# Kernel tuning notes

Measured on AMD Instinct MI355X. Metric: run time of the kernel, lower is better.

Reference implementation:

```python
import jax, jax.numpy as jnp
import numpy as np

B, N, C = 2, 2048, 1024
H = 16
HS = C // H
SCALE = HS ** -0.5


def setup_inputs() -> dict:
    key = jax.random.key(0)
    k1, k2, k3 = jax.random.split(key, 3)
    x = jax.random.normal(k1, (B, N, C), dtype=jnp.float32)
    # torch nn.Linear weights: (out_features, in_features)
    w_qkv = jax.random.normal(k2, (3 * C, C), dtype=jnp.float32) * (C ** -0.5)
    w_out = jax.random.normal(k3, (C, C), dtype=jnp.float32) * (C ** -0.5)
    b_out = jnp.zeros((C,), dtype=jnp.float32)
    return {"x": x, "w_qkv": w_qkv, "w_out": w_out, "b_out": b_out}


def reference(x, w_qkv, w_out, b_out):
    b, n, c = x.shape
    # qkv projection: (B,N,3C); original reshapes to (B,N,C,3) so q/k/v are
    # INTERLEAVED columns of the 3C output (stride-3 split), reproduced here.
    qkv = jnp.einsum('bnc,dc->bnd', x, w_qkv).reshape(b, n, c, 3)
    q = qkv[..., 0].reshape(b, n, H, HS).transpose(0, 2, 1, 3)  # (B,H,N,HS)
    k = qkv[..., 1].reshape(b, n, H, HS).transpose(0, 2, 1, 3)
    v = qkv[..., 2].reshape(b, n, H, HS).transpose(0, 2, 1, 3)
    scores = SCALE * jnp.einsum('bhnd,bhmd->bhnm', q, k)  # (B,H,N,N)
    weights = jax.nn.softmax(scores, axis=-1)  # dropout rate 0 -> identity
    attn = jnp.einsum('bhnm,bhmd->bhnd', weights, v)
    attn = attn.transpose(0, 2, 1, 3).reshape(b, n, c)
    return attn @ w_out.T + b_out
```

## Files before the change

### kernel.cpp

```cpp
#include <hip/hip_runtime.h>
#include <hip/hip_bf16.h>


typedef __attribute__((ext_vector_type(8))) short bfx8;
typedef __attribute__((ext_vector_type(4))) short bfx4;
typedef __attribute__((ext_vector_type(4))) float f32x4;

#define B_ 2
#define N_ 2048
#define C_ 1024
#define H_ 16
#define HS_ 64
#define M_TOT 4096
#define QKV_N 3072

__device__ __forceinline__ ushort f2bf(float f) {
  union { float f; unsigned u; } v; v.f = f;
  unsigned r = v.u + 0x7FFFu + ((v.u >> 16) & 1u);
  return (ushort)(r >> 16);
}

__device__ __forceinline__ void gload_lds16(const ushort* g, ushort* l) {
  __builtin_amdgcn_global_load_lds(
      (const __attribute__((address_space(1))) unsigned int*)g,
      (__attribute__((address_space(3))) unsigned int*)l, 16, 0, 0);
}

__device__ __forceinline__ uint32_t lds_addr(const ushort* p) {
  return (uint32_t)(size_t)(__attribute__((address_space(3))) const ushort*)p;
}

__global__ void convert_kernel(const float4* __restrict__ x,
                               const float4* __restrict__ wqkv,
                               const float4* __restrict__ wout,
                               ushort* __restrict__ xb,
                               ushort* __restrict__ wqkvb,
                               ushort* __restrict__ woutb) {
  const int NX = (M_TOT * C_) / 4;
  const int NW = (QKV_N * C_) / 4;
  const int NO = (C_ * C_) / 4;
  const int total = NX + NW + NO;
  const int stride = gridDim.x * blockDim.x;
  for (int i = blockIdx.x * blockDim.x + threadIdx.x; i < total; i += stride) {
    if (i < NX) {
      float4 v = x[i];
      ushort4 o; o.x = f2bf(v.x); o.y = f2bf(v.y); o.z = f2bf(v.z); o.w = f2bf(v.w);
      *(ushort4*)(xb + (size_t)i * 4) = o;
    } else if (i < NX + NW) {
      int q = i - NX;
      float4 v = wqkv[q];
      int e = q * 4;
      int j = e >> 10, col = e & 1023;
      int jp = ((j % 3) << 10) + (j / 3);
      ushort4 o; o.x = f2bf(v.x); o.y = f2bf(v.y); o.z = f2bf(v.z); o.w = f2bf(v.w);
      *(ushort4*)(wqkvb + ((size_t)jp << 10) + col) = o;
    } else {
      int q = i - NX - NW;
      float4 v = wout[q];
      ushort4 o; o.x = f2bf(v.x); o.y = f2bf(v.y); o.z = f2bf(v.z); o.w = f2bf(v.w);
      *(ushort4*)(woutb + (size_t)q * 4) = o;
    }
  }
}

template<int STORE_BF16>
__global__ __launch_bounds__(256)
void gemm_bt(const ushort* __restrict__ A, const ushort* __restrict__ Bm,
             ushort* __restrict__ Cb, float* __restrict__ Cf,
             const float* __restrict__ bias, int M, int N, int K) {
  __shared__ ushort As[128 * 64];
  __shared__ ushort Bs[128 * 64];
  const int tid = threadIdx.x;
  const int wave = tid >> 6, lane = tid & 63;
  const int l16 = lane & 15, lq = lane >> 4;
  const int brow = blockIdx.y * 128, bcol = blockIdx.x * 128;
  const int wr = (wave >> 1) * 64, wc = (wave & 1) * 64;

  f32x4 acc[4][4];
#pragma unroll
  for (int m = 0; m < 4; ++m)
#pragma unroll
    for (int n = 0; n < 4; ++n) acc[m][n] = f32x4{0.f, 0.f, 0.f, 0.f};

  for (int k0 = 0; k0 < K; k0 += 64) {
    __syncthreads();
#pragma unroll
    for (int r = 0; r < 4; ++r) {
      int off = (r * 256 + tid) * 8;
      gload_lds16(A + (size_t)(brow + (off >> 6)) * K + k0 + (off & 63), As + off);
    }
#pragma unroll
    for (int r = 0; r < 4; ++r) {
      int off = (r * 256 + tid) * 8;
      gload_lds16(Bm + (size_t)(bcol + (off >> 6)) * K + k0 + (off & 63), Bs + off);
    }
    asm volatile("s_waitcnt vmcnt(0)" ::: "memory");
    __syncthreads();
#pragma unroll
    for (int kk = 0; kk < 64; kk += 32) {
      bfx8 a[4], b[4];
#pragma unroll
      for (int m = 0; m < 4; ++m)
        a[m] = *(const bfx8*)(As + (wr + m * 16 + l16) * 64 + kk + lq * 8);
#pragma unroll
      for (int n = 0; n < 4; ++n)
        b[n] = *(const bfx8*)(Bs + (wc + n * 16 + l16) * 64 + kk + lq * 8);
#pragma unroll
      for (int m = 0; m < 4; ++m)
#pragma unroll
        for (int n = 0; n < 4; ++n)
          acc[m][n] = __builtin_amdgcn_mfma_f32_16x16x32_bf16(a[m], b[n], acc[m][n], 0, 0, 0);
    }
  }
#pragma unroll
  for (int m = 0; m < 4; ++m)
#pragma unroll
    for (int n = 0; n < 4; ++n)
#pragma unroll
      for (int r = 0; r < 4; ++r) {
        int grow = brow + wr + m * 16 + lq * 4 + r;
        int gcol = bcol + wc + n * 16 + l16;
        if (STORE_BF16) {
          Cb[(size_t)grow * N + gcol] = f2bf(acc[m][n][r]);
        } else {
          Cf[(size_t)grow * N + gcol] = acc[m][n][r] + bias[gcol];
        }
      }
}

__global__ __launch_bounds__(256)
void attn_kernel(const ushort* __restrict__ qkv, ushort* __restrict__ outb) {
  __shared__ ushort Ks[2][64 * 64];
  __shared__ ushort Vs[2][64 * 64];
  __shared__ ushort Ps[4][16 * 64];
  const int tid = threadIdx.x, wave = tid >> 6, lane = tid & 63;
  const int l16 = lane & 15, lq = lane >> 4;
  const int bh = blockIdx.y, b = bh >> 4, h = bh & 15;
  const int q0 = blockIdx.x * 64;
  const size_t RS = QKV_N;
  const ushort* Qb = qkv + ((size_t)(b * N_ + q0)) * RS + h * HS_;
  const ushort* Kb = qkv + ((size_t)(b * N_)) * RS + C_ + h * HS_;
  const ushort* Vb = qkv + ((size_t)(b * N_)) * RS + 2 * C_ + h * HS_;

  const int kRow = lane >> 3;
  const int kCol = (((lane & 7) ^ (lane >> 3)) << 3);
  const int vJ = ((lane >> 5) << 2) + ((lane & 7) >> 1);
  const int vD = ((lane >> 3) & 3) * 16 + (lane & 1) * 8;

  bfx8 qf0, qf1;
  {
    const ushort* qrow = Qb + (size_t)(wave * 16 + l16) * RS + lq * 8;
    qf0 = *(const bfx8*)(qrow);
    qf1 = *(const bfx8*)(qrow + 32);
  }

  const float CL = 0.125f * 1.44269504f;
  float m2 = -1e30f, l_s = 0.f;
  f32x4 o[4];
#pragma unroll
  for (int dt = 0; dt < 4; ++dt) o[dt] = f32x4{0.f, 0.f, 0.f, 0.f};

#define STAGE_TILE(KT, BUF)                                                     \
  {                                                                             \
    const ushort* kbase = Kb + (size_t)((KT) * 64) * RS;                        \
    const ushort* vbase = Vb + (size_t)((KT) * 64) * RS;                        \
    _Pragma("unroll")                                                           \
    for (int t = 0; t < 2; ++t) {                                               \
      int it = wave * 2 + t;                                                    \
      gload_lds16(kbase + (size_t)(it * 8 + kRow) * RS + kCol,                  \
                  &Ks[BUF][it * 512]);                                          \
      gload_lds16(vbase + (size_t)(it * 8 + vJ) * RS + vD,                      \
                  &Vs[BUF][it * 512]);                                          \
    }                                                                           \
  }

  STAGE_TILE(0, 0);
  __syncthreads();
  int cur = 0;
  const int pkey = (l16 & 7) << 3;
  ushort* Pw = Ps[wave];

  for (int kt = 0; kt < N_ / 64; ++kt) {
    if (kt + 1 < N_ / 64) STAGE_TILE(kt + 1, cur ^ 1);

    f32x4 s[4];
    const ushort* Kc = Ks[cur];
#pragma unroll
    for (int jt = 0; jt < 4; ++jt) {
      int row = jt * 16 + l16, swz = l16 & 7;
      const ushort* kr = Kc + row * 64;
      bfx8 kv0 = *(const bfx8*)(kr + ((lq ^ swz) << 3));
      bfx8 kv1 = *(const bfx8*)(kr + (((lq + 4) ^ swz) << 3));
      f32x4 z = {0.f, 0.f, 0.f, 0.f};
      z = __builtin_amdgcn_mfma_f32_16x16x32_bf16(kv0, qf0, z, 0, 0, 0);
      z = __builtin_amdgcn_mfma_f32_16x16x32_bf16(kv1, qf1, z, 0, 0, 0);
      s[jt] = z;
    }

    float t8[8];
#pragma unroll
    for (int i = 0; i < 8; ++i)
      t8[i] = fmaxf(s[i >> 1][(i & 1) * 2], s[i >> 1][(i & 1) * 2 + 1]);
    float t40 = fmaxf(t8[0], t8[1]), t41 = fmaxf(t8[2], t8[3]);
    float t42 = fmaxf(t8[4], t8[5]), t43 = fmaxf(t8[6], t8[7]);
    float tmax2 = fmaxf(fmaxf(t40, t41), fmaxf(t42, t43)) * CL;
    tmax2 = fmaxf(tmax2, __shfl_xor(tmax2, 16));
    tmax2 = fmaxf(tmax2, __shfl_xor(tmax2, 32));

    if (!__all(tmax2 <= m2 + 8.0f)) {
      float mn2 = fmaxf(m2, tmax2);
      float darg = m2 - mn2, sc;
      asm("v_exp_f32 %0, %1" : "=v"(sc) : "v"(darg));
      m2 = mn2;
      l_s *= sc;
      float sco[4];
#pragma unroll
      for (int r = 0; r < 4; ++r) sco[r] = __shfl(sc, (lane & 48) + lq * 4 + r);
#pragma unroll
      for (int dt = 0; dt < 4; ++dt)
#pragma unroll
        for (int r = 0; r < 4; ++r) o[dt][r] *= sco[r];
    }

    float tsum = 0.f;
#pragma unroll
    for (int jt = 0; jt < 4; ++jt) {
      float p[4];
#pragma unroll
      for (int r = 0; r < 4; ++r) {
        float a = __builtin_fmaf(s[jt][r], CL, -m2);
        asm("v_exp_f32 %0, %1" : "=v"(p[r]) : "v"(a));
      }
      tsum += (p[0] + p[1]) + (p[2] + p[3]);
      unsigned pk0, pk1;
      asm("v_cvt_pk_bf16_f32 %0, %1, %2" : "=v"(pk0) : "v"(p[0]), "v"(p[1]));
      asm("v_cvt_pk_bf16_f32 %0, %1, %2" : "=v"(pk1) : "v"(p[2]), "v"(p[3]));
      *(uint2*)(Pw + l16 * 64 + ((jt * 16 + lq * 4) ^ pkey)) = make_uint2(pk0, pk1);
    }
    l_s += tsum;

    asm volatile("s_waitcnt lgkmcnt(0)" ::: "memory");
    __builtin_amdgcn_sched_barrier(0);
    bfx8 pa0 = *(const bfx8*)(Pw + l16 * 64 + ((lq * 8) ^ pkey));
    bfx8 pa1 = *(const bfx8*)(Pw + l16 * 64 + ((32 + lq * 8) ^ pkey));

    uint32_t vbase = lds_addr(&Vs[cur][0]) + (uint32_t)(lq * 1024 + l16 * 8);
#pragma unroll
    for (int kk = 0; kk < 2; ++kk) {
      bfx4 t[8];
#pragma unroll
      for (int dt = 0; dt < 4; ++dt)
#pragma unroll
        for (int hf = 0; hf < 2; ++hf) {
          uint32_t a = vbase + (uint32_t)(kk * 4096 + hf * 512 + dt * 128);
          asm volatile("ds_read_b64_tr_b16 %0, %1" : "=v"(t[dt * 2 + hf]) : "v"(a));
        }
      asm volatile("s_waitcnt lgkmcnt(0)" ::: "memory");
      __builtin_amdgcn_sched_barrier(0);
      bfx8 pa = kk ? pa1 : pa0;
#pragma unroll
      for (int dt = 0; dt < 4; ++dt) {
        bfx8 vf = __builtin_shufflevector(t[dt * 2], t[dt * 2 + 1],
                                          0, 1, 2, 3, 4, 5, 6, 7);
        o[dt] = __builtin_amdgcn_mfma_f32_16x16x32_bf16(pa, vf, o[dt], 0, 0, 0);
      }
    }
    __syncthreads();
    cur ^= 1;
  }
#undef STAGE_TILE

  l_s += __shfl_xor(l_s, 16);
  l_s += __shfl_xor(l_s, 32);
  float inv = 1.0f / l_s;
  float linv[4];
#pragma unroll
  for (int r = 0; r < 4; ++r) linv[r] = __shfl(inv, (lane & 48) + lq * 4 + r);
#pragma unroll
  for (int dt = 0; dt < 4; ++dt)
#pragma unroll
    for (int r = 0; r < 4; ++r) {
      int n = q0 + wave * 16 + lq * 4 + r;
      int col = h * HS_ + dt * 16 + l16;
      outb[(size_t)(b * N_ + n) * C_ + col] = f2bf(o[dt][r] * linv[r]);
    }
}

extern "C" void kernel_launch(void* const* d_in, const int* in_sizes, int n_in,
                              void* d_out, int out_size, void* d_ws, size_t ws_size,
                              hipStream_t stream) {
  const float* x    = (const float*)d_in[0];
  const float* wqkv = (const float*)d_in[1];
  const float* wout = (const float*)d_in[2];
  const float* bout = (const float*)d_in[3];
  float* out = (float*)d_out;

  ushort* xb    = (ushort*)d_ws;
  ushort* wqkvb = xb + (size_t)M_TOT * C_;
  ushort* woutb = wqkvb + (size_t)QKV_N * C_;
  ushort* qkvb  = woutb + (size_t)C_ * C_;
  ushort* attnb = qkvb + (size_t)M_TOT * QKV_N;

  convert_kernel<<<2048, 256, 0, stream>>>((const float4*)x, (const float4*)wqkv,
                                           (const float4*)wout, xb, wqkvb, woutb);
  dim3 g1(QKV_N / 128, M_TOT / 128);
  gemm_bt<1><<<g1, 256, 0, stream>>>(xb, wqkvb, qkvb, nullptr, nullptr, M_TOT, QKV_N, C_);
  dim3 g2(N_ / 64, B_ * H_);
  attn_kernel<<<g2, 256, 0, stream>>>(qkvb, attnb);
  dim3 g3(C_ / 128, M_TOT / 128);
  gemm_bt<0><<<g3, 256, 0, stream>>>(attnb, woutb, nullptr, out, bout, M_TOT, C_, C_);
}
```

Baseline: 222.7 us.

## Replace QKV projection GEMM with 256x256-tile double-buffered 8-wave kernel

Adds a new GEMM kernel for the QKV projection. It uses 256x256 output tiles, 512 threads, XOR-swizzled LDS and double-buffered direct global-to-LDS loads. MFMA phases are interleaved with LDS fragment reads under barriers and setprio, and blocks are remapped for XCD-aware tile placement. The aim is higher data reuse and better overlap of memory with matrix math than the 128x128 kernel it replaces. In exchange it needs 128KB of dynamic LDS and launches only 192 blocks, which may leave the 256 CUs partly underused.

```diff
diff --git a/kernel.cpp b/kernel.cpp
--- a/kernel.cpp
+++ b/kernel.cpp
@@ -63,6 +63,153 @@
   }
 }
 
+__global__ __launch_bounds__(512, 2)
+void gemm256(const ushort* __restrict__ A, const ushort* __restrict__ Bm,
+             ushort* __restrict__ Cb, int M, int N, int K) {
+  extern __shared__ ushort LDSU[];
+  const int tid = threadIdx.x;
+  const int wave = tid >> 6, lane = tid & 63;
+  const int l16 = lane & 15, lq = lane >> 4;
+  const int wm = wave >> 2, wn = wave & 3;
+
+  const int cpx = gridDim.x >> 3;
+  const int tile = (blockIdx.x & 7) * cpx + (blockIdx.x >> 3);
+  const int nbx = N >> 8;
+  const int brow = (tile / nbx) << 8, bcol = (tile % nbx) << 8;
+
+  const int srow = tid >> 3;
+  const int scol = ((tid * 8) & 63) ^ ((srow & 7) << 3);
+  const ushort* Ab = A + (size_t)(brow + srow) * K + scol;
+  const ushort* Bb = Bm + (size_t)(bcol + srow) * K + scol;
+  const int sdst = tid * 8;
+
+  f32x4 acc[8][4];
+#pragma unroll
+  for (int m = 0; m < 8; ++m)
+#pragma unroll
+    for (int n = 0; n < 4; ++n) acc[m][n] = f32x4{0.f, 0.f, 0.f, 0.f};
+
+  const int key = (l16 & 7) << 3;
+  const int aRowBase = wm * 128 + l16;
+  const int bRowBase = wn * 64 + l16;
+
+#define STAGE(KT, BUF)                                                        \
+  {                                                                           \
+    const ushort* a_ = Ab + (KT) * 64;                                        \
+    const ushort* b_ = Bb + (KT) * 64;                                        \
+    ushort* al_ = &LDSU[(BUF) * 16384 + sdst];                                \
+    ushort* bl_ = &LDSU[32768 + (BUF) * 16384 + sdst];                        \
+    _Pragma("unroll")                                                         \
+    for (int i_ = 0; i_ < 4; ++i_) {                                          \
+      gload_lds16(a_ + (size_t)(i_ * 64) * K, al_ + i_ * 4096);               \
+      gload_lds16(b_ + (size_t)(i_ * 64) * K, bl_ + i_ * 4096);               \
+    }                                                                         \
+  }
+#define RD_A(dst, mf, ks, BUF)                                                \
+  dst = *(const bfx8*)&LDSU[(BUF) * 16384 + (aRowBase + (mf) * 16) * 64 +     \
+                            ((((ks) * 32) + lq * 8) ^ key)];
+#define RD_B(dst, nf, ks, BUF)                                                \
+  dst = *(const bfx8*)&LDSU[32768 + (BUF) * 16384 +                           \
+                            (bRowBase + (nf) * 16) * 64 +                     \
+                            ((((ks) * 32) + lq * 8) ^ key)];
+
+  STAGE(0, 0);
+  asm volatile("s_waitcnt vmcnt(0)" ::: "memory");
+  __syncthreads();
+
+  const int NT = K >> 6;
+  bfx8 af[8], b0[4], b1[4];
+#pragma unroll 1
+  for (int kt = 0; kt < NT; ++kt) {
+    const int buf = kt & 1;
+#pragma unroll
+    for (int mf = 0; mf < 4; ++mf)
+#pragma unroll
+      for (int ks = 0; ks < 2; ++ks) RD_A(af[mf * 2 + ks], mf, ks, buf);
+#pragma unroll
+    for (int nf = 0; nf < 2; ++nf)
+#pragma unroll
+      for (int ks = 0; ks < 2; ++ks) RD_B(b0[nf * 2 + ks], nf, ks, buf);
+    if (kt + 1 < NT) STAGE(kt + 1, buf ^ 1);
+    __builtin_amdgcn_s_barrier();
+    asm volatile("s_waitcnt lgkmcnt(0)" ::: "memory");
+    __builtin_amdgcn_sched_barrier(0);
+    __builtin_amdgcn_s_setprio(1);
+#pragma unroll
+    for (int mf = 0; mf < 4; ++mf)
+#pragma unroll
+      for (int nf = 0; nf < 2; ++nf)
+#pragma unroll
+        for (int ks = 0; ks < 2; ++ks)
+          acc[mf][nf] = __builtin_amdgcn_mfma_f32_16x16x32_bf16(
+              af[mf * 2 + ks], b0[nf * 2 + ks], acc[mf][nf], 0, 0, 0);
+    __builtin_amdgcn_s_setprio(0);
+    __builtin_amdgcn_s_barrier();
+#pragma unroll
+    for (int nf = 0; nf < 2; ++nf)
+#pragma unroll
+      for (int ks = 0; ks < 2; ++ks) RD_B(b1[nf * 2 + ks], nf + 2, ks, buf);
+    __builtin_amdgcn_s_barrier();
+    asm volatile("s_waitcnt lgkmcnt(0)" ::: "memory");
+    __builtin_amdgcn_sched_barrier(0);
+    __builtin_amdgcn_s_setprio(1);
+#pragma unroll
+    for (int mf = 0; mf < 4; ++mf)
+#pragma unroll
+      for (int nf = 0; nf < 2; ++nf)
+#pragma unroll
+        for (int ks = 0; ks < 2; ++ks)
+          acc[mf][nf + 2] = __builtin_amdgcn_mfma_f32_16x16x32_bf16(
+              af[mf * 2 + ks], b1[nf * 2 + ks], acc[mf][nf + 2], 0, 0, 0);
+    __builtin_amdgcn_s_setprio(0);
+    __builtin_amdgcn_s_barrier();
+#pragma unroll
+    for (int mf = 0; mf < 4; ++mf)
+#pragma unroll
+      for (int ks = 0; ks < 2; ++ks) RD_A(af[mf * 2 + ks], mf + 4, ks, buf);
+    __builtin_amdgcn_s_barrier();
+    asm volatile("s_waitcnt lgkmcnt(0)" ::: "memory");
+    __builtin_amdgcn_sched_barrier(0);
+    __builtin_amdgcn_s_setprio(1);
+#pragma unroll
+    for (int mf = 0; mf < 4; ++mf)
+#pragma unroll
+      for (int nf = 0; nf < 2; ++nf)
+#pragma unroll
+        for (int ks = 0; ks < 2; ++ks)
+          acc[mf + 4][nf + 2] = __builtin_amdgcn_mfma_f32_16x16x32_bf16(
+              af[mf * 2 + ks], b1[nf * 2 + ks], acc[mf + 4][nf + 2], 0, 0, 0);
+    __builtin_amdgcn_s_setprio(0);
+    __builtin_amdgcn_s_barrier();
+    __builtin_amdgcn_s_setprio(1);
+#pragma unroll
+    for (int mf = 0; mf < 4; ++mf)
+#pragma unroll
+      for (int nf = 0; nf < 2; ++nf)
+#pragma unroll
+        for (int ks = 0; ks < 2; ++ks)
+          acc[mf + 4][nf] = __builtin_amdgcn_mfma_f32_16x16x32_bf16(
+              af[mf * 2 + ks], b0[nf * 2 + ks], acc[mf + 4][nf], 0, 0, 0);
+    __builtin_amdgcn_s_setprio(0);
+    asm volatile("s_waitcnt vmcnt(0)" ::: "memory");
+    __builtin_amdgcn_s_barrier();
+  }
+#undef STAGE
+#undef RD_A
+#undef RD_B
+
+#pragma unroll
+  for (int mf = 0; mf < 8; ++mf)
+#pragma unroll
+    for (int nf = 0; nf < 4; ++nf)
+#pragma unroll
+      for (int r = 0; r < 4; ++r) {
+        int grow = brow + wm * 128 + mf * 16 + lq * 4 + r;
+        int gcol = bcol + wn * 64 + nf * 16 + l16;
+        Cb[(size_t)grow * N + gcol] = f2bf(acc[mf][nf][r]);
+      }
+}
+
 template<int STORE_BF16>
 __global__ __launch_bounds__(256)
 void gemm_bt(const ushort* __restrict__ A, const ushort* __restrict__ Bm,
@@ -301,10 +448,12 @@
   ushort* qkvb  = woutb + (size_t)C_ * C_;
   ushort* attnb = qkvb + (size_t)M_TOT * QKV_N;
 
+  hipFuncSetAttribute((const void*)gemm256,
+                      hipFuncAttributeMaxDynamicSharedMemorySize, 131072);
+
   convert_kernel<<<2048, 256, 0, stream>>>((const float4*)x, (const float4*)wqkv,
                                            (const float4*)wout, xb, wqkvb, woutb);
-  dim3 g1(QKV_N / 128, M_TOT / 128);
-  gemm_bt<1><<<g1, 256, 0, stream>>>(xb, wqkvb, qkvb, nullptr, nullptr, M_TOT, QKV_N, C_);
+  gemm256<<<192, 512, 131072, stream>>>(xb, wqkvb, qkvb, M_TOT, QKV_N, C_);
   dim3 g2(N_ / 64, B_ * H_);
   attn_kernel<<<g2, 256, 0, stream>>>(qkvb, attnb);
   dim3 g3(C_ / 128, M_TOT / 128);
```

New measurement: 210.2 us. -5.6%, faster.
